# Kernel optimization log

Measured on AMD Instinct MI355X. Metric: run time of the kernel, lower is better.

The kernel has to match this reference:

```python
import jax, jax.numpy as jnp
import numpy as np

B, S, D, L = 16, 2048, 256, 4  # batch, seq, embedding_dim, num_blocks
NUM_FEATS = 6  # time features; +1 price = 7 input channels


def _layernorm(x, g, b):
    mu = x.mean(-1, keepdims=True)
    var = x.var(-1, keepdims=True)
    return (x - mu) * jax.lax.rsqrt(var + 1e-5) * g + b


def _slstm(gx, Wh):
    """sLSTM with exponential gating + max stabilizer.
    gx: [S, B, 4D] input-side pre-activations; Wh: [D, 4D] recurrent weights.
    Returns hidden states [S, B, D]."""
    d = Wh.shape[0]
    b = gx.shape[1]
    z0 = jnp.zeros((b, d), gx.dtype)
    init = (z0, z0, z0, z0)  # c, n, h, m

    def step(carry, gx_t):
        c, n, h, m = carry
        g = gx_t + h @ Wh
        i_t, f_t, z_t, o_t = jnp.split(g, 4, axis=-1)
        m_new = jnp.maximum(f_t + m, i_t)          # stabilizer state
        i_p = jnp.exp(i_t - m_new)                 # exp input gate
        f_p = jnp.exp(f_t + m - m_new)             # exp forget gate
        c = f_p * c + i_p * jnp.tanh(z_t)
        n = f_p * n + i_p                          # normalizer
        h = jax.nn.sigmoid(o_t) * c / jnp.maximum(jnp.abs(n), 1.0)
        return (c, n, h, m_new), h

    _, hs = jax.lax.scan(step, init, gx)
    return hs


def setup_inputs() -> dict:
    key = jax.random.key(0)
    ks = jax.random.split(key, 10)
    s = 0.02
    return {
        "x": jax.random.normal(ks[0], (B, S), jnp.float32),
        "time_features": jax.random.normal(ks[1], (B, S, NUM_FEATS), jnp.float32),
        "in_W": jax.random.normal(ks[2], (NUM_FEATS + 1, D), jnp.float32) * s,
        "in_b": jnp.zeros((D,), jnp.float32),
        "ln_g": jnp.ones((L, D), jnp.float32),
        "ln_b": jnp.zeros((L, D), jnp.float32),
        "Wx": jax.random.normal(ks[3], (L, D, 4 * D), jnp.float32) * s,
        "Wh": jax.random.normal(ks[4], (L, D, 4 * D), jnp.float32) * s,
        "bg": jnp.zeros((L, 4 * D), jnp.float32),
        "fc_W": jax.random.normal(ks[5], (D, 1), jnp.float32) * s,
        "fc_b": jnp.zeros((1,), jnp.float32),
    }


def reference(x, time_features, in_W, in_b, ln_g, ln_b, Wx, Wh, bg, fc_W, fc_b):
    # concat price + time features -> [B, S, 7]; project to embedding_dim
    feats = jnp.concatenate([x[..., None], time_features], axis=-1)
    h = feats @ in_W + in_b  # [B, S, D]
    nblocks = ln_g.shape[0]
    for l in range(nblocks):  # fixed small layer count
        xn = _layernorm(h, ln_g[l], ln_b[l])
        gx = jnp.einsum("bsd,de->bse", xn, Wx[l]) + bg[l]  # [B,S,4D]
        hs = _slstm(gx.transpose(1, 0, 2), Wh[l])          # [S,B,D]
        h = h + hs.transpose(1, 0, 2)                       # residual
    # dropout is identity in eval mode
    return h[:, -1, :] @ fc_W + fc_b  # [B, 1]
```

## Files before the change

kernel.cpp:

```cpp
#include <hip/hip_runtime.h>

#define BB 16
#define SS 2048
#define DD 256
#define ND4 1024
#define PRD 16
#define PGD 8
#define HLP 4

typedef __attribute__((ext_vector_type(8))) _Float16 half8;
typedef __attribute__((ext_vector_type(4))) float f32x4;
typedef unsigned long long u64;
union H8 { half8 v; unsigned int u[4]; uint4 q; };

__device__ __forceinline__ u64 aload(const u64* p) {
    return __hip_atomic_load(p, __ATOMIC_RELAXED, __HIP_MEMORY_SCOPE_AGENT);
}
__device__ __forceinline__ void astore(u64* p, u64 v) {
    __hip_atomic_store(p, v, __ATOMIC_RELAXED, __HIP_MEMORY_SCOPE_AGENT);
}
__device__ __forceinline__ unsigned pload(const unsigned* p) {
    return __hip_atomic_load(p, __ATOMIC_RELAXED, __HIP_MEMORY_SCOPE_AGENT);
}
__device__ __forceinline__ void pstore(unsigned* p, unsigned v) {
    __hip_atomic_store(p, v, __ATOMIC_RELAXED, __HIP_MEMORY_SCOPE_AGENT);
}
__device__ __forceinline__ int aflag(int* p) {
    return __hip_atomic_load(p, __ATOMIC_RELAXED, __HIP_MEMORY_SCOPE_AGENT);
}
__device__ __forceinline__ void sflag(int* p) {
    __hip_atomic_store(p, 1, __ATOMIC_RELAXED, __HIP_MEMORY_SCOPE_AGENT);
}
__device__ __forceinline__ unsigned short f16b(float x) {
    union { _Float16 h; unsigned short u; } c; c.h = (_Float16)x; return c.u;
}
__device__ __forceinline__ bool spinBail(int& guard, int* af) {
    if ((++guard & 63) == 0) {
        __builtin_amdgcn_s_sleep(1);
        if (guard > (1 << 18) || aflag(af)) { sflag(af); return true; }
    }
    return false;
}

__global__ void embed_kernel(const float* __restrict__ x, const float* __restrict__ tf,
                             const float* __restrict__ inW, const float* __restrict__ inb,
                             float* __restrict__ h) {
    int tok = blockIdx.x, d = threadIdx.x;
    float xv = x[tok];
    float acc = inb[d] + xv * inW[d];
#pragma unroll
    for (int c = 0; c < 6; ++c)
        acc = fmaf(tf[tok * 6 + c], inW[(c + 1) * DD + d], acc);
    h[(size_t)tok * DD + d] = acc;
}

__global__ void wxprep_kernel(const float* __restrict__ Wx, unsigned short* __restrict__ Wxh) {
    int l = blockIdx.x >> 6, G = blockIdx.x & 63;
    int lane = threadIdx.x, quad = lane >> 4, mm = lane & 15;
    const float* W = Wx + (size_t)l * DD * ND4;
    unsigned short* o = Wxh + (size_t)blockIdx.x * 4096;
#pragma unroll
    for (int kc = 0; kc < 8; ++kc) {
        __align__(16) unsigned short tmp[8];
#pragma unroll
        for (int i = 0; i < 8; ++i)
            tmp[i] = f16b(W[(size_t)(kc * 32 + quad * 8 + i) * ND4 + G * 16 + mm]);
        *(uint4*)(o + ((size_t)kc * 64 + lane) * 8) = *(uint4*)tmp;
    }
}

__global__ __launch_bounds__(256, 1) void mega_kernel(
    const float* __restrict__ hemb, const float* __restrict__ Wh,
    const float* __restrict__ lng, const float* __restrict__ lnb,
    const float* __restrict__ bgp, const unsigned short* __restrict__ Wxh,
    float* __restrict__ hout,
    u64* __restrict__ Xbuf, u64* __restrict__ Rbuf, u64* __restrict__ GXbuf,
    unsigned* __restrict__ prog, int* __restrict__ abortFlag) {
    __shared__ __align__(16) char smemBlob[57344];
    const int bid = blockIdx.x;
    const int tid = threadIdx.x;

    if (bid < 64) {
        const int l = bid >> 4, g = bid & 15;
        const int w = tid >> 6, lane = tid & 63;
        const int mm = lane & 15, quad = lane >> 4;
        const int sb = tid >> 4, sd = tid & 15;
        const int dglob = g * 16 + sd;
        float (*gbuf)[4][16][16] = (float (*)[4][16][16])smemBlob;

        H8 bfr[8];
        {
            const float* WhL = Wh + (size_t)l * DD * ND4;
            const int col = w * 256 + g * 16 + mm;
#pragma unroll
            for (int kc = 0; kc < 8; ++kc)
#pragma unroll
                for (int p = 0; p < 4; ++p) {
                    float f0 = WhL[(size_t)(32 * kc + 8 * quad + 2 * p) * ND4 + col];
                    float f1 = WhL[(size_t)(32 * kc + 8 * quad + 2 * p + 1) * ND4 + col];
                    bfr[kc].u[p] = (unsigned)f16b(f0) | ((unsigned)f16b(f1) << 16);
                }
        }

        float c_ = 0.f, n_ = 0.f, m_ = 0.f;

        u64* Xl = Xbuf + (size_t)l * 4096;
        const u64* Rprev = Rbuf + (size_t)(l > 0 ? l - 1 : 0) * PRD * 4096;
        u64* Rcur = Rbuf + (size_t)(l < 3 ? l : 0) * PRD * 4096;
        const u64* GXl = GXbuf + (size_t)l * PGD * 16384;

        const int pquad = (dglob >> 3) & 3;
        const int ppair = (sd >> 1) & 3;
        const size_t pubIdx = (size_t)(g >> 1) * 256 + (size_t)pquad * 64 + (size_t)sb * 4 + ppair;
        const bool doPub = (sd & 1) == 0;
        const size_t rdBase = (size_t)quad * 64 + (size_t)mm * 4;
        const size_t gxIdx = (size_t)sb * 1024 + dglob;
        const size_t rIdx = (size_t)sb * 256 + dglob;
        const float* hemb0 = hemb + (size_t)sb * SS * DD + dglob;
        float* hrow = hout + (size_t)sb * SS * DD + dglob;
        __syncthreads();

        for (int t = 0; t < SS; ++t) {
            const unsigned tagT = (unsigned)(t + 1);
            float gxi, gxf, gxz, gxoo, hin;
            {
                const u64* Gp = GXl + (size_t)(t & (PGD - 1)) * 16384 + gxIdx;
                const u64* Rp = Rprev + (size_t)(t & (PRD - 1)) * 4096 + rIdx;
                u64 a0, a1, a2, a3, ar = 0;
                int guard = 0;
                for (;;) {
                    a0 = aload(Gp); a1 = aload(Gp + 256);
                    a2 = aload(Gp + 512); a3 = aload(Gp + 768);
                    if (l > 0) ar = aload(Rp);
                    bool ok = ((unsigned)(a0 >> 32) == tagT) & ((unsigned)(a1 >> 32) == tagT) &
                              ((unsigned)(a2 >> 32) == tagT) & ((unsigned)(a3 >> 32) == tagT) &
                              ((l == 0) | ((unsigned)(ar >> 32) == tagT));
                    if (ok) break;
                    if (spinBail(guard, abortFlag)) break;
                }
                gxi = __uint_as_float((unsigned)a0);
                gxf = __uint_as_float((unsigned)a1);
                gxz = __uint_as_float((unsigned)a2);
                gxoo = __uint_as_float((unsigned)a3);
                hin = (l > 0) ? __uint_as_float((unsigned)ar) : hemb0[(size_t)t * DD];
            }
            f32x4 acc0 = {0.f, 0.f, 0.f, 0.f}, acc1 = {0.f, 0.f, 0.f, 0.f};
            if (t > 0) {
                const unsigned tag = (unsigned)t;
                u64* Xp = Xl + (size_t)(t & 1) * 2048;
                u64 v[32];
                int guard = 0;
                for (;;) {
#pragma unroll
                    for (int kc = 0; kc < 8; ++kc)
#pragma unroll
                        for (int p = 0; p < 4; ++p)
                            v[kc * 4 + p] = aload(Xp + (size_t)kc * 256 + rdBase + p);
                    bool ok = true;
#pragma unroll
                    for (int i = 0; i < 32; ++i) ok &= ((unsigned)(v[i] >> 32) == tag);
                    if (ok) break;
                    if ((++guard & 255) == 0) {
                        if (guard > (1 << 18) || aflag(abortFlag)) { sflag(abortFlag); break; }
                    }
                }
                H8 afr[8];
#pragma unroll
                for (int kc = 0; kc < 8; ++kc)
#pragma unroll
                    for (int p = 0; p < 4; ++p) afr[kc].u[p] = (unsigned)v[kc * 4 + p];
                acc0 = __builtin_amdgcn_mfma_f32_16x16x32_f16(afr[0].v, bfr[0].v, acc0, 0, 0, 0);
                acc1 = __builtin_amdgcn_mfma_f32_16x16x32_f16(afr[1].v, bfr[1].v, acc1, 0, 0, 0);
                acc0 = __builtin_amdgcn_mfma_f32_16x16x32_f16(afr[2].v, bfr[2].v, acc0, 0, 0, 0);
                acc1 = __builtin_amdgcn_mfma_f32_16x16x32_f16(afr[3].v, bfr[3].v, acc1, 0, 0, 0);
                acc0 = __builtin_amdgcn_mfma_f32_16x16x32_f16(afr[4].v, bfr[4].v, acc0, 0, 0, 0);
                acc1 = __builtin_amdgcn_mfma_f32_16x16x32_f16(afr[5].v, bfr[5].v, acc1, 0, 0, 0);
                acc0 = __builtin_amdgcn_mfma_f32_16x16x32_f16(afr[6].v, bfr[6].v, acc0, 0, 0, 0);
                acc1 = __builtin_amdgcn_mfma_f32_16x16x32_f16(afr[7].v, bfr[7].v, acc1, 0, 0, 0);
            }
            f32x4 acc = acc0 + acc1;
            const int par = t & 1;
#pragma unroll
            for (int r = 0; r < 4; ++r) gbuf[par][w][quad * 4 + r][mm] = acc[r];
            __syncthreads();
            float gi = gbuf[par][0][sb][sd] + gxi;
            float gf = gbuf[par][1][sb][sd] + gxf;
            float gz = gbuf[par][2][sb][sd] + gxz;
            float go = gbuf[par][3][sb][sd] + gxoo;
            float mn = fmaxf(gf + m_, gi);
            float ip = __expf(gi - mn);
            float fp = __expf(gf + m_ - mn);
            float e2z = __expf(2.f * gz);
            float th = 1.f - 2.f * __builtin_amdgcn_rcpf(e2z + 1.f);
            c_ = fp * c_ + ip * th;
            n_ = fp * n_ + ip;
            m_ = mn;
            float sg = __builtin_amdgcn_rcpf(1.f + __expf(-go));
            float hval = sg * c_ * __builtin_amdgcn_rcpf(fmaxf(fabsf(n_), 1.f));
            float rnew = hin + hval;
            if (l == 3) {
                hrow[(size_t)t * DD] = rnew;
            } else {
                if (t >= PRD) {
                    unsigned needT = (unsigned)(t - PRD);
                    const unsigned* ps = prog + (l + 1);
                    const unsigned* pg = prog + 4 + (l + 1) * 4 + (int)(needT & (HLP - 1));
                    int guard = 0;
                    while (!((pload(ps) >= needT + 2) && (pload(pg) >= needT + 1))) {
                        if (spinBail(guard, abortFlag)) break;
                    }
                }
                astore(Rcur + (size_t)(t & (PRD - 1)) * 4096 + rIdx,
                       ((u64)tagT << 32) | (u64)__float_as_uint(rnew));
            }
            float hodd = __shfl_down(hval, 1);
            if (doPub) {
                unsigned payload = (unsigned)f16b(hval) | ((unsigned)f16b(hodd) << 16);
                astore(Xl + (size_t)((t + 1) & 1) * 2048 + pubIdx, ((u64)tagT << 32) | payload);
            }
            __syncthreads();
            if (g == 0 && tid == 0) pstore(prog + l, (unsigned)(t + 1));
        }
    } else {
        const int hix = bid - 64;
        const int l = hix >> 2;
        const int j = hix & 3;
        const int w = tid >> 6, lane = tid & 63;
        const int mm = lane & 15, quad = lane >> 4;
        const int hb_ = tid >> 4, hd0 = (tid & 15) * 16;
        unsigned short (*hA)[264] = (unsigned short (*)[264])smemBlob;

        const u64* Rin = Rbuf + (size_t)(l > 0 ? l - 1 : 0) * PRD * 4096;
        u64* GXl = GXbuf + (size_t)l * PGD * 16384;
        const unsigned short* WxL = Wxh + (size_t)l * 262144;
        const float* lngL = lng + l * DD;
        const float* lnbL = lnb + l * DD;
        const float* bgL = bgp + (size_t)l * ND4;
        unsigned* myProg = prog + 4 + l * 4 + j;
        const unsigned* scanProg = prog + l;

        for (int t = j; t < SS; t += HLP) {
            const unsigned tagT = (unsigned)(t + 1);
            float rv[16];
            if (l == 0) {
                const float4* p = (const float4*)(hemb + ((size_t)hb_ * SS + t) * DD + hd0);
#pragma unroll
                for (int q4 = 0; q4 < 4; ++q4) {
                    float4 f = p[q4];
                    rv[q4 * 4 + 0] = f.x; rv[q4 * 4 + 1] = f.y;
                    rv[q4 * 4 + 2] = f.z; rv[q4 * 4 + 3] = f.w;
                }
            } else {
                const u64* Rp = Rin + (size_t)(t & (PRD - 1)) * 4096 + (size_t)tid * 16;
                int guard = 0;
                for (;;) {
                    u64 vv[16];
#pragma unroll
                    for (int i = 0; i < 16; ++i) vv[i] = aload(Rp + i);
                    bool ok = true;
#pragma unroll
                    for (int i = 0; i < 16; ++i) ok &= ((unsigned)(vv[i] >> 32) == tagT);
                    if (ok) {
#pragma unroll
                        for (int i = 0; i < 16; ++i) rv[i] = __uint_as_float((unsigned)vv[i]);
                        break;
                    }
                    if (spinBail(guard, abortFlag)) {
#pragma unroll
                        for (int i = 0; i < 16; ++i) rv[i] = 0.f;
                        break;
                    }
                }
            }
            float s = 0.f, ssq = 0.f;
#pragma unroll
            for (int i = 0; i < 16; ++i) { s += rv[i]; ssq += rv[i] * rv[i]; }
#pragma unroll
            for (int msk = 1; msk < 16; msk <<= 1) {
                s += __shfl_xor(s, msk);
                ssq += __shfl_xor(ssq, msk);
            }
            float muv = s * (1.f / 256.f);
            float rsv = rsqrtf(fmaxf(ssq * (1.f / 256.f) - muv * muv, 0.f) + 1e-5f);
            {
                __align__(16) unsigned short ov[16];
#pragma unroll
                for (int i = 0; i < 16; ++i)
                    ov[i] = f16b((rv[i] - muv) * rsv * lngL[hd0 + i] + lnbL[hd0 + i]);
                *(uint4*)&hA[hb_][hd0] = *(uint4*)&ov[0];
                *(uint4*)&hA[hb_][hd0 + 8] = *(uint4*)&ov[8];
            }
            __syncthreads();
            H8 A[8];
#pragma unroll
            for (int kc = 0; kc < 8; ++kc)
                A[kc].q = *(const uint4*)&hA[mm][kc * 32 + quad * 8];
            f32x4 acc[16];
            const unsigned short* WxW = WxL + (size_t)w * 16 * 4096;
#pragma unroll
            for (int n = 0; n < 16; ++n) {
                const unsigned short* bp = WxW + (size_t)n * 4096 + (size_t)lane * 8;
                f32x4 a = {0.f, 0.f, 0.f, 0.f};
#pragma unroll
                for (int kc = 0; kc < 8; ++kc) {
                    H8 B;
                    B.q = *(const uint4*)(bp + (size_t)kc * 512);
                    a = __builtin_amdgcn_mfma_f32_16x16x32_f16(A[kc].v, B.v, a, 0, 0, 0);
                }
                acc[n] = a;
            }
            if (t >= PGD) {
                unsigned need = (unsigned)(t - PGD) + 2;
                int guard = 0;
                while (pload(scanProg) < need) {
                    if (spinBail(guard, abortFlag)) break;
                }
            }
            u64* Gq = GXl + (size_t)(t & (PGD - 1)) * 16384;
#pragma unroll
            for (int n = 0; n < 16; ++n) {
                int c = (w * 16 + n) * 16 + mm;
                float bgv = bgL[c];
                f32x4 a = acc[n];
#pragma unroll
                for (int r = 0; r < 4; ++r)
                    astore(Gq + (size_t)(quad * 4 + r) * 1024 + c,
                           ((u64)tagT << 32) | (u64)__float_as_uint(a[r] + bgv));
            }
            __syncthreads();
            if (tid == 0) pstore(myProg, (unsigned)(t + 1));
        }
    }
}

__global__ void final_kernel(const float* __restrict__ h, const float* __restrict__ fcW,
                             const float* __restrict__ fcb, float* __restrict__ out) {
    int b = blockIdx.x, lane = threadIdx.x;
    const float4 hv = *(const float4*)(h + ((size_t)b * SS + (SS - 1)) * DD + lane * 4);
    const float4 wv = *(const float4*)(fcW + lane * 4);
    float s = hv.x * wv.x + hv.y * wv.y + hv.z * wv.z + hv.w * wv.w;
#pragma unroll
    for (int off = 32; off; off >>= 1) s += __shfl_down(s, off);
    if (lane == 0) out[b] = s + fcb[0];
}

extern "C" void kernel_launch(void* const* d_in, const int* in_sizes, int n_in,
                              void* d_out, int out_size, void* d_ws, size_t ws_size,
                              hipStream_t stream) {
    const float* x   = (const float*)d_in[0];
    const float* tf  = (const float*)d_in[1];
    const float* inW = (const float*)d_in[2];
    const float* inb = (const float*)d_in[3];
    const float* lng = (const float*)d_in[4];
    const float* lnb = (const float*)d_in[5];
    const float* Wx  = (const float*)d_in[6];
    const float* Wh  = (const float*)d_in[7];
    const float* bg  = (const float*)d_in[8];
    const float* fcW = (const float*)d_in[9];
    const float* fcb = (const float*)d_in[10];
    float* out = (float*)d_out;

    const size_t nTok = (size_t)BB * SS;
    float* hemb = (float*)d_ws;
    float* hout = hemb + nTok * DD;
    unsigned short* Wxh = (unsigned short*)(hout + nTok * DD);
    u64* Xbuf = (u64*)(Wxh + 1048576);
    u64* Rbuf = Xbuf + 4 * 2 * 2048;
    u64* GXbuf = Rbuf + 3 * PRD * 4096;
    unsigned* prog = (unsigned*)(GXbuf + 4 * PGD * 16384);
    int* abortFlag = (int*)(prog + 20);

    const size_t needed = (size_t)((char*)(abortFlag + 1) - (char*)d_ws);
    if (ws_size < needed) return;

    hipMemsetAsync(prog, 0, 20 * sizeof(unsigned) + sizeof(int), stream);

    embed_kernel<<<nTok, DD, 0, stream>>>(x, tf, inW, inb, hemb);
    wxprep_kernel<<<4 * 64, 64, 0, stream>>>(Wx, Wxh);
    mega_kernel<<<80, 256, 0, stream>>>(hemb, Wh, lng, lnb, bg, Wxh, hout,
                                        Xbuf, Rbuf, GXbuf, prog, abortFlag);
    final_kernel<<<BB, 64, 0, stream>>>(hout, fcW, fcb, out);
    (void)in_sizes; (void)n_in; (void)out_size;
}
```

Baseline: 7.233 ms.

## Overlap gate-input loads with MFMA, drop per-step barrier, cache progress counters

In the recurrent scan blocks, the gate-input and residual atomic loads are now issued at the start of each step, and their tags are checked only after the recurrent MFMAs, so load latency overlaps the matmul. The hidden-state fp16 publish moves ahead of the residual back-pressure wait, and the trailing per-step __syncthreads is removed; the double-buffered gbuf, now padded to 17 columns to avoid LDS bank conflicts, makes the single barrier sufficient. Consumer-progress counters are cached in registers, and the four helper counters are polled together as a minimum, so most steps skip spinning on global flags. The risk is subtler memory-ordering assumptions around the progress flag once the end-of-step barrier is gone.

```diff
diff --git a/kernel.cpp b/kernel.cpp
--- a/kernel.cpp
+++ b/kernel.cpp
@@ -86,7 +86,7 @@
         const int mm = lane & 15, quad = lane >> 4;
         const int sb = tid >> 4, sd = tid & 15;
         const int dglob = g * 16 + sd;
-        float (*gbuf)[4][16][16] = (float (*)[4][16][16])smemBlob;
+        float (*gbuf)[4][16][17] = (float (*)[4][16][17])smemBlob;
 
         H8 bfr[8];
         {
@@ -118,32 +118,21 @@
         const size_t rIdx = (size_t)sb * 256 + dglob;
         const float* hemb0 = hemb + (size_t)sb * SS * DD + dglob;
         float* hrow = hout + (size_t)sb * SS * DD + dglob;
+        const unsigned* psP = prog + (l + 1);
+        const unsigned* pgP = prog + 4 + (l + 1) * 4;
+        unsigned psC = 0, pgMinC = 0;
         __syncthreads();
 
         for (int t = 0; t < SS; ++t) {
             const unsigned tagT = (unsigned)(t + 1);
-            float gxi, gxf, gxz, gxoo, hin;
-            {
-                const u64* Gp = GXl + (size_t)(t & (PGD - 1)) * 16384 + gxIdx;
-                const u64* Rp = Rprev + (size_t)(t & (PRD - 1)) * 4096 + rIdx;
-                u64 a0, a1, a2, a3, ar = 0;
-                int guard = 0;
-                for (;;) {
-                    a0 = aload(Gp); a1 = aload(Gp + 256);
-                    a2 = aload(Gp + 512); a3 = aload(Gp + 768);
-                    if (l > 0) ar = aload(Rp);
-                    bool ok = ((unsigned)(a0 >> 32) == tagT) & ((unsigned)(a1 >> 32) == tagT) &
-                              ((unsigned)(a2 >> 32) == tagT) & ((unsigned)(a3 >> 32) == tagT) &
-                              ((l == 0) | ((unsigned)(ar >> 32) == tagT));
-                    if (ok) break;
-                    if (spinBail(guard, abortFlag)) break;
-                }
-                gxi = __uint_as_float((unsigned)a0);
-                gxf = __uint_as_float((unsigned)a1);
-                gxz = __uint_as_float((unsigned)a2);
-                gxoo = __uint_as_float((unsigned)a3);
-                hin = (l > 0) ? __uint_as_float((unsigned)ar) : hemb0[(size_t)t * DD];
-            }
+            const u64* Gp = GXl + (size_t)(t & (PGD - 1)) * 16384 + gxIdx;
+            const u64* Rp = Rprev + (size_t)(t & (PRD - 1)) * 4096 + rIdx;
+            u64 a0 = aload(Gp), a1 = aload(Gp + 256);
+            u64 a2 = aload(Gp + 512), a3 = aload(Gp + 768);
+            u64 ar = 0;
+            if (l > 0) ar = aload(Rp);
+            float hembv = (l == 0) ? hemb0[(size_t)t * DD] : 0.f;
+
             f32x4 acc0 = {0.f, 0.f, 0.f, 0.f}, acc1 = {0.f, 0.f, 0.f, 0.f};
             if (t > 0) {
                 const unsigned tag = (unsigned)t;
@@ -179,10 +168,31 @@
                 acc1 = __builtin_amdgcn_mfma_f32_16x16x32_f16(afr[7].v, bfr[7].v, acc1, 0, 0, 0);
             }
             f32x4 acc = acc0 + acc1;
+
+            {
+                int guard = 0;
+                for (;;) {
+                    bool ok = ((unsigned)(a0 >> 32) == tagT) & ((unsigned)(a1 >> 32) == tagT) &
+                              ((unsigned)(a2 >> 32) == tagT) & ((unsigned)(a3 >> 32) == tagT) &
+                              ((l == 0) | ((unsigned)(ar >> 32) == tagT));
+                    if (ok) break;
+                    if (spinBail(guard, abortFlag)) break;
+                    a0 = aload(Gp); a1 = aload(Gp + 256);
+                    a2 = aload(Gp + 512); a3 = aload(Gp + 768);
+                    if (l > 0) ar = aload(Rp);
+                }
+            }
+            float gxi = __uint_as_float((unsigned)a0);
+            float gxf = __uint_as_float((unsigned)a1);
+            float gxz = __uint_as_float((unsigned)a2);
+            float gxoo = __uint_as_float((unsigned)a3);
+            float hin = (l > 0) ? __uint_as_float((unsigned)ar) : hembv;
+
             const int par = t & 1;
 #pragma unroll
             for (int r = 0; r < 4; ++r) gbuf[par][w][quad * 4 + r][mm] = acc[r];
             __syncthreads();
+
             float gi = gbuf[par][0][sb][sd] + gxi;
             float gf = gbuf[par][1][sb][sd] + gxf;
             float gz = gbuf[par][2][sb][sd] + gxz;
@@ -197,28 +207,36 @@
             m_ = mn;
             float sg = __builtin_amdgcn_rcpf(1.f + __expf(-go));
             float hval = sg * c_ * __builtin_amdgcn_rcpf(fmaxf(fabsf(n_), 1.f));
+
+            float hodd = __shfl_down(hval, 1);
+            if (doPub) {
+                unsigned payload = (unsigned)f16b(hval) | ((unsigned)f16b(hodd) << 16);
+                astore(Xl + (size_t)((t + 1) & 1) * 2048 + pubIdx, ((u64)tagT << 32) | payload);
+            }
+
             float rnew = hin + hval;
             if (l == 3) {
                 hrow[(size_t)t * DD] = rnew;
             } else {
                 if (t >= PRD) {
                     unsigned needT = (unsigned)(t - PRD);
-                    const unsigned* ps = prog + (l + 1);
-                    const unsigned* pg = prog + 4 + (l + 1) * 4 + (int)(needT & (HLP - 1));
-                    int guard = 0;
-                    while (!((pload(ps) >= needT + 2) && (pload(pg) >= needT + 1))) {
-                        if (spinBail(guard, abortFlag)) break;
+                    if (!(psC >= needT + 2 && pgMinC >= needT + 1)) {
+                        int guard = 0;
+                        for (;;) {
+                            psC = pload(psP);
+                            unsigned p0 = pload(pgP), p1 = pload(pgP + 1);
+                            unsigned p2 = pload(pgP + 2), p3 = pload(pgP + 3);
+                            unsigned mn01 = p0 < p1 ? p0 : p1;
+                            unsigned mn23 = p2 < p3 ? p2 : p3;
+                            pgMinC = mn01 < mn23 ? mn01 : mn23;
+                            if (psC >= needT + 2 && pgMinC >= needT + 1) break;
+                            if (spinBail(guard, abortFlag)) break;
+                        }
                     }
                 }
                 astore(Rcur + (size_t)(t & (PRD - 1)) * 4096 + rIdx,
                        ((u64)tagT << 32) | (u64)__float_as_uint(rnew));
             }
-            float hodd = __shfl_down(hval, 1);
-            if (doPub) {
-                unsigned payload = (unsigned)f16b(hval) | ((unsigned)f16b(hodd) << 16);
-                astore(Xl + (size_t)((t + 1) & 1) * 2048 + pubIdx, ((u64)tagT << 32) | payload);
-            }
-            __syncthreads();
             if (g == 0 && tid == 0) pstore(prog + l, (unsigned)(t + 1));
         }
     } else {
@@ -238,6 +256,7 @@
         const float* bgL = bgp + (size_t)l * ND4;
         unsigned* myProg = prog + 4 + l * 4 + j;
         const unsigned* scanProg = prog + l;
+        unsigned spC = 0;
 
         for (int t = j; t < SS; t += HLP) {
             const unsigned tagT = (unsigned)(t + 1);
@@ -311,9 +330,13 @@
             }
             if (t >= PGD) {
                 unsigned need = (unsigned)(t - PGD) + 2;
-                int guard = 0;
-                while (pload(scanProg) < need) {
-                    if (spinBail(guard, abortFlag)) break;
+                if (spC < need) {
+                    int guard = 0;
+                    for (;;) {
+                        spC = pload(scanProg);
+                        if (spC >= need) break;
+                        if (spinBail(guard, abortFlag)) break;
+                    }
                 }
             }
             u64* Gq = GXl + (size_t)(t & (PGD - 1)) * 16384;
```

Measured after the change: 7.771 ms. +7.4%, slower.

## Fuse input projection into recurrent blocks, folding LayerNorm affine into Wx

Applied to the files above, without the earlier changes.

Drops the 16 separate input-projection helper blocks and the GX staging buffer. Each recurrent block now computes its own slice of x@Wx per timestep with MFMA, using register-resident fp16 Wx fragments, alongside the recurrent h@Wh product. LayerNorm gamma is folded into Wx and beta into the gate bias in prep kernels. The next layer receives residuals as packed fp16 in MFMA fragment layout, plus an fp32 copy for the residual add. This removes a cross-block handoff and its polling from each step, at the cost of extra MFMA and LayerNorm work on the serial critical path and fp16 rounding of the LayerNorm input.

```diff
diff --git a/kernel.cpp b/kernel.cpp
--- a/kernel.cpp
+++ b/kernel.cpp
@@ -5,13 +5,11 @@
 #define DD 256
 #define ND4 1024
 #define PRD 16
-#define PGD 8
-#define HLP 4
 
 typedef __attribute__((ext_vector_type(8))) _Float16 half8;
 typedef __attribute__((ext_vector_type(4))) float f32x4;
 typedef unsigned long long u64;
-union H8 { half8 v; unsigned int u[4]; uint4 q; };
+union H8 { half8 v; unsigned u[4]; uint4 q; };
 
 __device__ __forceinline__ u64 aload(const u64* p) {
     return __hip_atomic_load(p, __ATOMIC_RELAXED, __HIP_MEMORY_SCOPE_AGENT);
@@ -54,282 +52,244 @@
     h[(size_t)tok * DD + d] = acc;
 }
 
-__global__ void wxprep_kernel(const float* __restrict__ Wx, unsigned short* __restrict__ Wxh) {
+__global__ void wprep_wh_kernel(const float* __restrict__ W, unsigned short* __restrict__ Wo) {
     int l = blockIdx.x >> 6, G = blockIdx.x & 63;
     int lane = threadIdx.x, quad = lane >> 4, mm = lane & 15;
-    const float* W = Wx + (size_t)l * DD * ND4;
-    unsigned short* o = Wxh + (size_t)blockIdx.x * 4096;
+    const float* Wl = W + (size_t)l * DD * ND4;
+    unsigned short* o = Wo + (size_t)blockIdx.x * 4096;
 #pragma unroll
     for (int kc = 0; kc < 8; ++kc) {
         __align__(16) unsigned short tmp[8];
 #pragma unroll
         for (int i = 0; i < 8; ++i)
-            tmp[i] = f16b(W[(size_t)(kc * 32 + quad * 8 + i) * ND4 + G * 16 + mm]);
+            tmp[i] = f16b(Wl[(size_t)(kc * 32 + quad * 8 + i) * ND4 + G * 16 + mm]);
         *(uint4*)(o + ((size_t)kc * 64 + lane) * 8) = *(uint4*)tmp;
     }
 }
 
+__global__ void wprep_wx_kernel(const float* __restrict__ W, const float* __restrict__ lng,
+                                unsigned short* __restrict__ Wo) {
+    int l = blockIdx.x >> 6, G = blockIdx.x & 63;
+    int lane = threadIdx.x, quad = lane >> 4, mm = lane & 15;
+    const float* Wl = W + (size_t)l * DD * ND4;
+    const float* gl = lng + l * DD;
+    unsigned short* o = Wo + (size_t)blockIdx.x * 4096;
+#pragma unroll
+    for (int kc = 0; kc < 8; ++kc) {
+        __align__(16) unsigned short tmp[8];
+#pragma unroll
+        for (int i = 0; i < 8; ++i) {
+            int k = kc * 32 + quad * 8 + i;
+            tmp[i] = f16b(gl[k] * Wl[(size_t)k * ND4 + G * 16 + mm]);
+        }
+        *(uint4*)(o + ((size_t)kc * 64 + lane) * 8) = *(uint4*)tmp;
+    }
+}
+
+__global__ void bgprep_kernel(const float* __restrict__ bg, const float* __restrict__ lnb,
+                              const float* __restrict__ Wx, float* __restrict__ bgp2) {
+    int idx = blockIdx.x * 256 + threadIdx.x;
+    int l = idx >> 10, col = idx & 1023;
+    const float* Wl = Wx + (size_t)l * DD * ND4;
+    const float* bl = lnb + l * DD;
+    float acc = bg[idx];
+    for (int d = 0; d < DD; ++d) acc = fmaf(bl[d], Wl[(size_t)d * ND4 + col], acc);
+    bgp2[idx] = acc;
+}
+
 __global__ __launch_bounds__(256, 1) void mega_kernel(
-    const float* __restrict__ hemb, const float* __restrict__ Wh,
-    const float* __restrict__ lng, const float* __restrict__ lnb,
-    const float* __restrict__ bgp, const unsigned short* __restrict__ Wxh,
+    const float* __restrict__ hemb, const unsigned short* __restrict__ Whh,
+    const unsigned short* __restrict__ Wxh, const float* __restrict__ bgp2,
     float* __restrict__ hout,
-    u64* __restrict__ Xbuf, u64* __restrict__ Rbuf, u64* __restrict__ GXbuf,
+    u64* __restrict__ Xbuf, u64* __restrict__ Rn, u64* __restrict__ Rf,
     unsigned* __restrict__ prog, int* __restrict__ abortFlag) {
-    __shared__ __align__(16) char smemBlob[57344];
+    __shared__ float gbuf[2][4][16][18];
     const int bid = blockIdx.x;
     const int tid = threadIdx.x;
-
-    if (bid < 64) {
-        const int l = bid >> 4, g = bid & 15;
-        const int w = tid >> 6, lane = tid & 63;
-        const int mm = lane & 15, quad = lane >> 4;
-        const int sb = tid >> 4, sd = tid & 15;
-        const int dglob = g * 16 + sd;
-        float (*gbuf)[4][16][16] = (float (*)[4][16][16])smemBlob;
-
-        H8 bfr[8];
-        {
-            const float* WhL = Wh + (size_t)l * DD * ND4;
-            const int col = w * 256 + g * 16 + mm;
+    const int l = bid >> 4, g = bid & 15;
+    const int w = tid >> 6, lane = tid & 63;
+    const int mm = lane & 15, quad = lane >> 4;
+    const int sb = tid >> 4, sd = tid & 15;
+    const int dglob = g * 16 + sd;
+
+    H8 bWh[8], bWx[8];
+    {
+        const unsigned short* ph = Whh + (size_t)(l * 64 + w * 16 + g) * 4096 + (size_t)lane * 8;
+        const unsigned short* px = Wxh + (size_t)(l * 64 + w * 16 + g) * 4096 + (size_t)lane * 8;
+#pragma unroll
+        for (int kc = 0; kc < 8; ++kc) {
+            bWh[kc].q = *(const uint4*)(ph + (size_t)kc * 512);
+            bWx[kc].q = *(const uint4*)(px + (size_t)kc * 512);
+        }
+    }
+    float bgv4[4];
+#pragma unroll
+    for (int gam = 0; gam < 4; ++gam) bgv4[gam] = bgp2[l * ND4 + gam * 256 + dglob];
+
+    float c_ = 0.f, n_ = 0.f, m_ = 0.f;
+
+    u64* Xl = Xbuf + (size_t)l * 2 * 2048;
+    u64* RnO = Rn + (size_t)l * PRD * 2048;
+    u64* RfO = Rf + (size_t)l * PRD * 4096;
+    const u64* RnI = Rn + (size_t)(l > 0 ? l - 1 : 0) * PRD * 2048;
+    const u64* RfI = Rf + (size_t)(l > 0 ? l - 1 : 0) * PRD * 4096;
+
+    const size_t pubIdx = (size_t)(g >> 1) * 256 + (size_t)((dglob >> 3) & 3) * 64 +
+                          (size_t)sb * 4 + ((sd >> 1) & 3);
+    const bool doPub = (sd & 1) == 0;
+    const size_t rdB = (size_t)quad * 64 + (size_t)mm * 4;
+    const size_t rfIdx = (size_t)sb * 256 + dglob;
+
+    const unsigned* consP = prog + (l + 1);
+    unsigned consC = 0;
+    unsigned* myProg = prog + l;
+    const float* hembRow = hemb + (size_t)mm * SS * DD;
+    const float* hembHin = hemb + (size_t)sb * SS * DD + dglob;
+    float* houtP = hout + (size_t)sb * SS * DD + dglob;
+    __syncthreads();
+
+    for (int t = 0; t < SS; ++t) {
+        const unsigned tagT = (unsigned)(t + 1);
+        H8 rfrag[8];
+        float hin;
+        if (l == 0) {
+            const float* hp = hembRow + (size_t)t * DD + quad * 8;
+#pragma unroll
+            for (int kc = 0; kc < 8; ++kc) {
+                float4 f0 = *(const float4*)(hp + kc * 32);
+                float4 f1 = *(const float4*)(hp + kc * 32 + 4);
+                rfrag[kc].v[0] = (_Float16)f0.x; rfrag[kc].v[1] = (_Float16)f0.y;
+                rfrag[kc].v[2] = (_Float16)f0.z; rfrag[kc].v[3] = (_Float16)f0.w;
+                rfrag[kc].v[4] = (_Float16)f1.x; rfrag[kc].v[5] = (_Float16)f1.y;
+                rfrag[kc].v[6] = (_Float16)f1.z; rfrag[kc].v[7] = (_Float16)f1.w;
+            }
+            hin = hembHin[(size_t)t * DD];
+        } else {
+            const u64* Rp = RnI + (size_t)(t & (PRD - 1)) * 2048;
+            const u64* Rfp = RfI + (size_t)(t & (PRD - 1)) * 4096 + rfIdx;
+            u64 v[32], hv;
+            int guard = 0;
+            for (;;) {
+#pragma unroll
+                for (int kc = 0; kc < 8; ++kc)
+#pragma unroll
+                    for (int p = 0; p < 4; ++p)
+                        v[kc * 4 + p] = aload(Rp + (size_t)kc * 256 + rdB + p);
+                hv = aload(Rfp);
+                bool ok = ((unsigned)(hv >> 32) == tagT);
+#pragma unroll
+                for (int i = 0; i < 32; ++i) ok &= ((unsigned)(v[i] >> 32) == tagT);
+                if (ok) break;
+                if (spinBail(guard, abortFlag)) break;
+            }
 #pragma unroll
             for (int kc = 0; kc < 8; ++kc)
 #pragma unroll
-                for (int p = 0; p < 4; ++p) {
-                    float f0 = WhL[(size_t)(32 * kc + 8 * quad + 2 * p) * ND4 + col];
-                    float f1 = WhL[(size_t)(32 * kc + 8 * quad + 2 * p + 1) * ND4 + col];
-                    bfr[kc].u[p] = (unsigned)f16b(f0) | ((unsigned)f16b(f1) << 16);
+                for (int p = 0; p < 4; ++p) rfrag[kc].u[p] = (unsigned)v[kc * 4 + p];
+            hin = __uint_as_float((unsigned)hv);
+        }
+        float s = 0.f, ss = 0.f;
+#pragma unroll
+        for (int kc = 0; kc < 8; ++kc)
+#pragma unroll
+            for (int i = 0; i < 8; ++i) {
+                float xv = (float)rfrag[kc].v[i];
+                s += xv; ss = fmaf(xv, xv, ss);
+            }
+        s += __shfl_xor(s, 16); ss += __shfl_xor(ss, 16);
+        s += __shfl_xor(s, 32); ss += __shfl_xor(ss, 32);
+        float mu = s * (1.f / 256.f);
+        float rs = rsqrtf(fmaxf(ss * (1.f / 256.f) - mu * mu, 0.f) + 1e-5f);
+        _Float16 muh = (_Float16)mu, rsh = (_Float16)rs;
+        half8 mus = {muh, muh, muh, muh, muh, muh, muh, muh};
+        half8 rss = {rsh, rsh, rsh, rsh, rsh, rsh, rsh, rsh};
+        f32x4 acc0 = {0.f, 0.f, 0.f, 0.f}, acc1 = {0.f, 0.f, 0.f, 0.f};
+#pragma unroll
+        for (int kc = 0; kc < 8; kc += 2) {
+            H8 z0, z1;
+            z0.v = (rfrag[kc].v - mus) * rss;
+            z1.v = (rfrag[kc + 1].v - mus) * rss;
+            acc0 = __builtin_amdgcn_mfma_f32_16x16x32_f16(z0.v, bWx[kc].v, acc0, 0, 0, 0);
+            acc1 = __builtin_amdgcn_mfma_f32_16x16x32_f16(z1.v, bWx[kc + 1].v, acc1, 0, 0, 0);
+        }
+        if (t > 0) {
+            const unsigned tg = (unsigned)t;
+            const u64* Xp = Xl + (size_t)(t & 1) * 2048;
+            u64 v[32];
+            int guard = 0;
+            for (;;) {
+#pragma unroll
+                for (int kc = 0; kc < 8; ++kc)
+#pragma unroll
+                    for (int p = 0; p < 4; ++p)
+                        v[kc * 4 + p] = aload(Xp + (size_t)kc * 256 + rdB + p);
+                bool ok = true;
+#pragma unroll
+                for (int i = 0; i < 32; ++i) ok &= ((unsigned)(v[i] >> 32) == tg);
+                if (ok) break;
+                if ((++guard & 127) == 0) {
+                    if (guard > (1 << 18) || aflag(abortFlag)) { sflag(abortFlag); break; }
                 }
-        }
-
-        float c_ = 0.f, n_ = 0.f, m_ = 0.f;
-
-        u64* Xl = Xbuf + (size_t)l * 4096;
-        const u64* Rprev = Rbuf + (size_t)(l > 0 ? l - 1 : 0) * PRD * 4096;
-        u64* Rcur = Rbuf + (size_t)(l < 3 ? l : 0) * PRD * 4096;
-        const u64* GXl = GXbuf + (size_t)l * PGD * 16384;
-
-        const int pquad = (dglob >> 3) & 3;
-        const int ppair = (sd >> 1) & 3;
-        const size_t pubIdx = (size_t)(g >> 1) * 256 + (size_t)pquad * 64 + (size_t)sb * 4 + ppair;
-        const bool doPub = (sd & 1) == 0;
-        const size_t rdBase = (size_t)quad * 64 + (size_t)mm * 4;
-        const size_t gxIdx = (size_t)sb * 1024 + dglob;
-        const size_t rIdx = (size_t)sb * 256 + dglob;
-        const float* hemb0 = hemb + (size_t)sb * SS * DD + dglob;
-        float* hrow = hout + (size_t)sb * SS * DD + dglob;
+            }
+            H8 afr[8];
+#pragma unroll
+            for (int kc = 0; kc < 8; ++kc)
+#pragma unroll
+                for (int p = 0; p < 4; ++p) afr[kc].u[p] = (unsigned)v[kc * 4 + p];
+#pragma unroll
+            for (int kc = 0; kc < 8; kc += 2) {
+                acc0 = __builtin_amdgcn_mfma_f32_16x16x32_f16(afr[kc].v, bWh[kc].v, acc0, 0, 0, 0);
+                acc1 = __builtin_amdgcn_mfma_f32_16x16x32_f16(afr[kc + 1].v, bWh[kc + 1].v, acc1, 0, 0, 0);
+            }
+        }
+        f32x4 acc = acc0 + acc1;
+        const int par = t & 1;
+#pragma unroll
+        for (int r = 0; r < 4; ++r) gbuf[par][w][quad * 4 + r][mm] = acc[r];
         __syncthreads();
-
-        for (int t = 0; t < SS; ++t) {
-            const unsigned tagT = (unsigned)(t + 1);
-            float gxi, gxf, gxz, gxoo, hin;
-            {
-                const u64* Gp = GXl + (size_t)(t & (PGD - 1)) * 16384 + gxIdx;
-                const u64* Rp = Rprev + (size_t)(t & (PRD - 1)) * 4096 + rIdx;
-                u64 a0, a1, a2, a3, ar = 0;
-                int guard = 0;
-                for (;;) {
-                    a0 = aload(Gp); a1 = aload(Gp + 256);
-                    a2 = aload(Gp + 512); a3 = aload(Gp + 768);
-                    if (l > 0) ar = aload(Rp);
-                    bool ok = ((unsigned)(a0 >> 32) == tagT) & ((unsigned)(a1 >> 32) == tagT) &
-                              ((unsigned)(a2 >> 32) == tagT) & ((unsigned)(a3 >> 32) == tagT) &
-                              ((l == 0) | ((unsigned)(ar >> 32) == tagT));
-                    if (ok) break;
-                    if (spinBail(guard, abortFlag)) break;
-                }
-                gxi = __uint_as_float((unsigned)a0);
-                gxf = __uint_as_float((unsigned)a1);
-                gxz = __uint_as_float((unsigned)a2);
-                gxoo = __uint_as_float((unsigned)a3);
-                hin = (l > 0) ? __uint_as_float((unsigned)ar) : hemb0[(size_t)t * DD];
-            }
-            f32x4 acc0 = {0.f, 0.f, 0.f, 0.f}, acc1 = {0.f, 0.f, 0.f, 0.f};
-            if (t > 0) {
-                const unsigned tag = (unsigned)t;
-                u64* Xp = Xl + (size_t)(t & 1) * 2048;
-                u64 v[32];
-                int guard = 0;
-                for (;;) {
-#pragma unroll
-                    for (int kc = 0; kc < 8; ++kc)
-#pragma unroll
-                        for (int p = 0; p < 4; ++p)
-                            v[kc * 4 + p] = aload(Xp + (size_t)kc * 256 + rdBase + p);
-                    bool ok = true;
-#pragma unroll
-                    for (int i = 0; i < 32; ++i) ok &= ((unsigned)(v[i] >> 32) == tag);
-                    if (ok) break;
-                    if ((++guard & 255) == 0) {
-                        if (guard > (1 << 18) || aflag(abortFlag)) { sflag(abortFlag); break; }
-                    }
-                }
-                H8 afr[8];
-#pragma unroll
-                for (int kc = 0; kc < 8; ++kc)
-#pragma unroll
-                    for (int p = 0; p < 4; ++p) afr[kc].u[p] = (unsigned)v[kc * 4 + p];
-                acc0 = __builtin_amdgcn_mfma_f32_16x16x32_f16(afr[0].v, bfr[0].v, acc0, 0, 0, 0);
-                acc1 = __builtin_amdgcn_mfma_f32_16x16x32_f16(afr[1].v, bfr[1].v, acc1, 0, 0, 0);
-                acc0 = __builtin_amdgcn_mfma_f32_16x16x32_f16(afr[2].v, bfr[2].v, acc0, 0, 0, 0);
-                acc1 = __builtin_amdgcn_mfma_f32_16x16x32_f16(afr[3].v, bfr[3].v, acc1, 0, 0, 0);
-                acc0 = __builtin_amdgcn_mfma_f32_16x16x32_f16(afr[4].v, bfr[4].v, acc0, 0, 0, 0);
-                acc1 = __builtin_amdgcn_mfma_f32_16x16x32_f16(afr[5].v, bfr[5].v, acc1, 0, 0, 0);
-                acc0 = __builtin_amdgcn_mfma_f32_16x16x32_f16(afr[6].v, bfr[6].v, acc0, 0, 0, 0);
-                acc1 = __builtin_amdgcn_mfma_f32_16x16x32_f16(afr[7].v, bfr[7].v, acc1, 0, 0, 0);
-            }
-            f32x4 acc = acc0 + acc1;
-            const int par = t & 1;
-#pragma unroll
-            for (int r = 0; r < 4; ++r) gbuf[par][w][quad * 4 + r][mm] = acc[r];
-            __syncthreads();
-            float gi = gbuf[par][0][sb][sd] + gxi;
-            float gf = gbuf[par][1][sb][sd] + gxf;
-            float gz = gbuf[par][2][sb][sd] + gxz;
-            float go = gbuf[par][3][sb][sd] + gxoo;
-            float mn = fmaxf(gf + m_, gi);
-            float ip = __expf(gi - mn);
-            float fp = __expf(gf + m_ - mn);
-            float e2z = __expf(2.f * gz);
-            float th = 1.f - 2.f * __builtin_amdgcn_rcpf(e2z + 1.f);
-            c_ = fp * c_ + ip * th;
-            n_ = fp * n_ + ip;
-            m_ = mn;
-            float sg = __builtin_amdgcn_rcpf(1.f + __expf(-go));
-            float hval = sg * c_ * __builtin_amdgcn_rcpf(fmaxf(fabsf(n_), 1.f));
-            float rnew = hin + hval;
-            if (l == 3) {
-                hrow[(size_t)t * DD] = rnew;
-            } else {
-                if (t >= PRD) {
-                    unsigned needT = (unsigned)(t - PRD);
-                    const unsigned* ps = prog + (l + 1);
-                    const unsigned* pg = prog + 4 + (l + 1) * 4 + (int)(needT & (HLP - 1));
+        float gi = gbuf[par][0][sb][sd] + bgv4[0];
+        float gf = gbuf[par][1][sb][sd] + bgv4[1];
+        float gz = gbuf[par][2][sb][sd] + bgv4[2];
+        float go = gbuf[par][3][sb][sd] + bgv4[3];
+        float mn = fmaxf(gf + m_, gi);
+        float ip = __expf(gi - mn);
+        float fp = __expf(gf + m_ - mn);
+        float e2z = __expf(2.f * gz);
+        float th = 1.f - 2.f * __builtin_amdgcn_rcpf(e2z + 1.f);
+        c_ = fp * c_ + ip * th;
+        n_ = fp * n_ + ip;
+        m_ = mn;
+        float sg = __builtin_amdgcn_rcpf(1.f + __expf(-go));
+        float hval = sg * c_ * __builtin_amdgcn_rcpf(fmaxf(fabsf(n_), 1.f));
+        float rnew = hin + hval;
+        float hodd = __shfl_down(hval, 1);
+        float rodd = __shfl_down(rnew, 1);
+        if (doPub) {
+            unsigned payX = (unsigned)f16b(hval) | ((unsigned)f16b(hodd) << 16);
+            astore(Xl + (size_t)((t + 1) & 1) * 2048 + pubIdx, ((u64)tagT << 32) | payX);
+        }
+        if (l == 3) {
+            houtP[(size_t)t * DD] = rnew;
+        } else {
+            if (t >= PRD) {
+                unsigned need = (unsigned)(t - PRD + 2);
+                if (consC < need) {
                     int guard = 0;
-                    while (!((pload(ps) >= needT + 2) && (pload(pg) >= needT + 1))) {
+                    for (;;) {
+                        consC = pload(consP);
+                        if (consC >= need) break;
                         if (spinBail(guard, abortFlag)) break;
                     }
                 }
-                astore(Rcur + (size_t)(t & (PRD - 1)) * 4096 + rIdx,
-                       ((u64)tagT << 32) | (u64)__float_as_uint(rnew));
-            }
-            float hodd = __shfl_down(hval, 1);
+            }
+            const size_t slot = (size_t)(t & (PRD - 1));
             if (doPub) {
-                unsigned payload = (unsigned)f16b(hval) | ((unsigned)f16b(hodd) << 16);
-                astore(Xl + (size_t)((t + 1) & 1) * 2048 + pubIdx, ((u64)tagT << 32) | payload);
-            }
-            __syncthreads();
-            if (g == 0 && tid == 0) pstore(prog + l, (unsigned)(t + 1));
-        }
-    } else {
-        const int hix = bid - 64;
-        const int l = hix >> 2;
-        const int j = hix & 3;
-        const int w = tid >> 6, lane = tid & 63;
-        const int mm = lane & 15, quad = lane >> 4;
-        const int hb_ = tid >> 4, hd0 = (tid & 15) * 16;
-        unsigned short (*hA)[264] = (unsigned short (*)[264])smemBlob;
-
-        const u64* Rin = Rbuf + (size_t)(l > 0 ? l - 1 : 0) * PRD * 4096;
-        u64* GXl = GXbuf + (size_t)l * PGD * 16384;
-        const unsigned short* WxL = Wxh + (size_t)l * 262144;
-        const float* lngL = lng + l * DD;
-        const float* lnbL = lnb + l * DD;
-        const float* bgL = bgp + (size_t)l * ND4;
-        unsigned* myProg = prog + 4 + l * 4 + j;
-        const unsigned* scanProg = prog + l;
-
-        for (int t = j; t < SS; t += HLP) {
-            const unsigned tagT = (unsigned)(t + 1);
-            float rv[16];
-            if (l == 0) {
-                const float4* p = (const float4*)(hemb + ((size_t)hb_ * SS + t) * DD + hd0);
-#pragma unroll
-                for (int q4 = 0; q4 < 4; ++q4) {
-                    float4 f = p[q4];
-                    rv[q4 * 4 + 0] = f.x; rv[q4 * 4 + 1] = f.y;
-                    rv[q4 * 4 + 2] = f.z; rv[q4 * 4 + 3] = f.w;
-                }
-            } else {
-                const u64* Rp = Rin + (size_t)(t & (PRD - 1)) * 4096 + (size_t)tid * 16;
-                int guard = 0;
-                for (;;) {
-                    u64 vv[16];
-#pragma unroll
-                    for (int i = 0; i < 16; ++i) vv[i] = aload(Rp + i);
-                    bool ok = true;
-#pragma unroll
-                    for (int i = 0; i < 16; ++i) ok &= ((unsigned)(vv[i] >> 32) == tagT);
-                    if (ok) {
-#pragma unroll
-                        for (int i = 0; i < 16; ++i) rv[i] = __uint_as_float((unsigned)vv[i]);
-                        break;
-                    }
-                    if (spinBail(guard, abortFlag)) {
-#pragma unroll
-                        for (int i = 0; i < 16; ++i) rv[i] = 0.f;
-                        break;
-                    }
-                }
-            }
-            float s = 0.f, ssq = 0.f;
-#pragma unroll
-            for (int i = 0; i < 16; ++i) { s += rv[i]; ssq += rv[i] * rv[i]; }
-#pragma unroll
-            for (int msk = 1; msk < 16; msk <<= 1) {
-                s += __shfl_xor(s, msk);
-                ssq += __shfl_xor(ssq, msk);
-            }
-            float muv = s * (1.f / 256.f);
-            float rsv = rsqrtf(fmaxf(ssq * (1.f / 256.f) - muv * muv, 0.f) + 1e-5f);
-            {
-                __align__(16) unsigned short ov[16];
-#pragma unroll
-                for (int i = 0; i < 16; ++i)
-                    ov[i] = f16b((rv[i] - muv) * rsv * lngL[hd0 + i] + lnbL[hd0 + i]);
-                *(uint4*)&hA[hb_][hd0] = *(uint4*)&ov[0];
-                *(uint4*)&hA[hb_][hd0 + 8] = *(uint4*)&ov[8];
-            }
-            __syncthreads();
-            H8 A[8];
-#pragma unroll
-            for (int kc = 0; kc < 8; ++kc)
-                A[kc].q = *(const uint4*)&hA[mm][kc * 32 + quad * 8];
-            f32x4 acc[16];
-            const unsigned short* WxW = WxL + (size_t)w * 16 * 4096;
-#pragma unroll
-            for (int n = 0; n < 16; ++n) {
-                const unsigned short* bp = WxW + (size_t)n * 4096 + (size_t)lane * 8;
-                f32x4 a = {0.f, 0.f, 0.f, 0.f};
-#pragma unroll
-                for (int kc = 0; kc < 8; ++kc) {
-                    H8 B;
-                    B.q = *(const uint4*)(bp + (size_t)kc * 512);
-                    a = __builtin_amdgcn_mfma_f32_16x16x32_f16(A[kc].v, B.v, a, 0, 0, 0);
-                }
-                acc[n] = a;
-            }
-            if (t >= PGD) {
-                unsigned need = (unsigned)(t - PGD) + 2;
-                int guard = 0;
-                while (pload(scanProg) < need) {
-                    if (spinBail(guard, abortFlag)) break;
-                }
-            }
-            u64* Gq = GXl + (size_t)(t & (PGD - 1)) * 16384;
-#pragma unroll
-            for (int n = 0; n < 16; ++n) {
-                int c = (w * 16 + n) * 16 + mm;
-                float bgv = bgL[c];
-                f32x4 a = acc[n];
-#pragma unroll
-                for (int r = 0; r < 4; ++r)
-                    astore(Gq + (size_t)(quad * 4 + r) * 1024 + c,
-                           ((u64)tagT << 32) | (u64)__float_as_uint(a[r] + bgv));
-            }
-            __syncthreads();
-            if (tid == 0) pstore(myProg, (unsigned)(t + 1));
-        }
+                unsigned payR = (unsigned)f16b(rnew) | ((unsigned)f16b(rodd) << 16);
+                astore(RnO + slot * 2048 + pubIdx, ((u64)tagT << 32) | payR);
+            }
+            astore(RfO + slot * 4096 + rfIdx, ((u64)tagT << 32) | (u64)__float_as_uint(rnew));
+        }
+        if (g == 0 && tid == 0) pstore(myProg, tagT);
     }
 }
 
@@ -364,21 +324,25 @@
     float* hemb = (float*)d_ws;
     float* hout = hemb + nTok * DD;
     unsigned short* Wxh = (unsigned short*)(hout + nTok * DD);
-    u64* Xbuf = (u64*)(Wxh + 1048576);
-    u64* Rbuf = Xbuf + 4 * 2 * 2048;
-    u64* GXbuf = Rbuf + 3 * PRD * 4096;
-    unsigned* prog = (unsigned*)(GXbuf + 4 * PGD * 16384);
-    int* abortFlag = (int*)(prog + 20);
+    unsigned short* Whh = Wxh + 1048576;
+    float* bgp2 = (float*)(Whh + 1048576);
+    u64* Xbuf = (u64*)(bgp2 + 4096);
+    u64* Rn = Xbuf + 4 * 2 * 2048;
+    u64* Rf = Rn + 3 * PRD * 2048;
+    unsigned* prog = (unsigned*)(Rf + 3 * PRD * 4096);
+    int* abortFlag = (int*)(prog + 8);
 
     const size_t needed = (size_t)((char*)(abortFlag + 1) - (char*)d_ws);
     if (ws_size < needed) return;
 
-    hipMemsetAsync(prog, 0, 20 * sizeof(unsigned) + sizeof(int), stream);
+    hipMemsetAsync(prog, 0, 8 * sizeof(unsigned) + sizeof(int), stream);
 
     embed_kernel<<<nTok, DD, 0, stream>>>(x, tf, inW, inb, hemb);
-    wxprep_kernel<<<4 * 64, 64, 0, stream>>>(Wx, Wxh);
-    mega_kernel<<<80, 256, 0, stream>>>(hemb, Wh, lng, lnb, bg, Wxh, hout,
-                                        Xbuf, Rbuf, GXbuf, prog, abortFlag);
+    wprep_wh_kernel<<<256, 64, 0, stream>>>(Wh, Whh);
+    wprep_wx_kernel<<<256, 64, 0, stream>>>(Wx, lng, Wxh);
+    bgprep_kernel<<<16, 256, 0, stream>>>(bg, lnb, Wx, bgp2);
+    mega_kernel<<<64, 256, 0, stream>>>(hemb, Whh, Wxh, bgp2, hout,
+                                        Xbuf, Rn, Rf, prog, abortFlag);
     final_kernel<<<BB, 64, 0, stream>>>(hout, fcW, fcb, out);
     (void)in_sizes; (void)n_in; (void)out_size;
 }
```

Result: slower. 9.391 ms (+29.8%).
